# Kernel optimization log

Hardware: AMD Instinct MI355X
Metric: run time of the kernel (lower is better)

Reference implementation:

```python
import jax, jax.numpy as jnp
import numpy as np

B, NA, D, H = 64, 32, 128, 6  # scenes, agents/scene, out_dim, heads
N = B * NA
E = B * NA * NA


def layer_norm(x, g, b, eps=1e-5):
    m = jnp.mean(x, axis=-1, keepdims=True)
    v = jnp.var(x, axis=-1, keepdims=True)
    return (x - m) * jax.lax.rsqrt(v + eps) * g + b


def setup_inputs() -> dict:
    key = jax.random.key(0)
    ks = jax.random.split(key, 10)
    # fully-connected edges within each scene
    ids = jnp.arange(N, dtype=jnp.int32).reshape(B, NA)
    hi = jnp.broadcast_to(ids[:, :, None], (B, NA, NA)).reshape(-1)  # repeat 'd -> (d n)'
    wi = jnp.broadcast_to(ids[:, None, :], (B, NA, NA)).reshape(-1)  # repeat 'd -> (n d)'
    s_in = 1.0 / np.sqrt(D)
    s_hd = 1.0 / np.sqrt(H * D)
    return {
        'agents': jax.random.normal(ks[0], (N, D), jnp.float32),
        'hi': hi, 'wi': wi,
        'Wq': jax.random.normal(ks[1], (H * D, D), jnp.float32) * s_in,
        'gq': jnp.ones((H * D,), jnp.float32), 'bq': jnp.zeros((H * D,), jnp.float32),
        'Wk': jax.random.normal(ks[2], (H * D, D), jnp.float32) * s_in,
        'gk': jnp.ones((H * D,), jnp.float32), 'bk': jnp.zeros((H * D,), jnp.float32),
        'Wv': jax.random.normal(ks[3], (H * D, D), jnp.float32) * s_in,
        'gv': jnp.ones((H * D,), jnp.float32), 'bv': jnp.zeros((H * D,), jnp.float32),
        'Wo1': jax.random.normal(ks[4], (D, H * D), jnp.float32) * s_hd,
        'go': jnp.ones((D,), jnp.float32), 'bo': jnp.zeros((D,), jnp.float32),
        'Wo2': jax.random.normal(ks[5], (D, D), jnp.float32) * s_in,
        'W1': jax.random.normal(ks[6], (D, D), jnp.float32) * s_in,
        'gn': jnp.ones((D,), jnp.float32), 'bn': jnp.zeros((D,), jnp.float32),
        'W2': jax.random.normal(ks[7], (D, D), jnp.float32) * s_in,
    }


def reference(agents, hi, wi, Wq, gq, bq, Wk, gk, bk, Wv, gv, bv, Wo1, go, bo, Wo2, W1, gn, bn, W2):
    n, d = agents.shape
    scale = d ** -0.5
    xh = agents[hi]                                   # [E, D]
    xw = agents[wi]                                   # [E, D]
    q = layer_norm(xh @ Wq.T, gq, bq).reshape(-1, H, d)                 # [E, H, D]
    k = layer_norm(xw @ Wk.T, gk, bk).reshape(-1, H, d)
    v = jax.nn.relu(layer_norm(xw @ Wv.T, gv, bv)).reshape(-1, H, d)
    att = jnp.sum(q * k, axis=-1) * scale             # [E, H] per-edge score
    att = jnp.exp(att - jnp.max(att))                 # global max, as in original
    att_sum = jax.ops.segment_sum(att, hi, num_segments=n)   # [N, H]
    att = att / att_sum[hi]
    out = jax.ops.segment_sum(att[..., None] * v, hi, num_segments=n)   # [N, H, D]
    out = out.reshape(n, H * d)
    out = jax.nn.relu(layer_norm(out @ Wo1.T, go, bo)) @ Wo2.T          # to_out
    nodes = agents @ W1.T
    nodes = jax.nn.relu(layer_norm(nodes + out, gn, bn))
    nodes = nodes @ W2.T
    return jax.nn.relu(nodes + agents)
```

## Files before the change

### kernel.cpp

```cpp
#include <hip/hip_runtime.h>
#include <math.h>

#define NN 2048
#define HH 6
#define HD 768
#define NA 32
#define NB 64

typedef __bf16 bf16x8 __attribute__((ext_vector_type(8)));
typedef float  f32x4  __attribute__((ext_vector_type(4)));

__device__ __forceinline__ void split2(float f, ushort& h, ushort& l) {
    const uint u = __float_as_uint(f);
    h = (ushort)(u >> 16);
    const float hf = __uint_as_float((uint)h << 16);
    l = (ushort)(__float_as_uint(f - hf) >> 16);
}

__device__ __forceinline__ bf16x8 pack8(const ushort* s) {
    uint4 u;
    u.x = (uint)s[0] | ((uint)s[1] << 16);
    u.y = (uint)s[2] | ((uint)s[3] << 16);
    u.z = (uint)s[4] | ((uint)s[5] << 16);
    u.w = (uint)s[6] | ((uint)s[7] << 16);
    return *(bf16x8*)&u;
}

__device__ __forceinline__ void ln8_split(
    const float* __restrict__ x, float mu, float rs,
    const float* __restrict__ g, const float* __restrict__ b,
    bf16x8& hi, bf16x8& lo)
{
    const float4 x0 = *(const float4*)x;
    const float4 x1 = *(const float4*)(x + 4);
    const float4 g0 = *(const float4*)g;
    const float4 g1 = *(const float4*)(g + 4);
    const float4 b0 = *(const float4*)b;
    const float4 b1 = *(const float4*)(b + 4);
    ushort hh[8], ll[8];
    float v;
    v = (x0.x - mu) * rs * g0.x + b0.x; split2(v, hh[0], ll[0]);
    v = (x0.y - mu) * rs * g0.y + b0.y; split2(v, hh[1], ll[1]);
    v = (x0.z - mu) * rs * g0.z + b0.z; split2(v, hh[2], ll[2]);
    v = (x0.w - mu) * rs * g0.w + b0.w; split2(v, hh[3], ll[3]);
    v = (x1.x - mu) * rs * g1.x + b1.x; split2(v, hh[4], ll[4]);
    v = (x1.y - mu) * rs * g1.y + b1.y; split2(v, hh[5], ll[5]);
    v = (x1.z - mu) * rs * g1.z + b1.z; split2(v, hh[6], ll[6]);
    v = (x1.w - mu) * rs * g1.w + b1.w; split2(v, hh[7], ll[7]);
    hi = pack8(hh); lo = pack8(ll);
}

__global__ __launch_bounds__(256) void split_kernel(
    const float* __restrict__ agents, const float* __restrict__ Wq,
    const float* __restrict__ Wk, const float* __restrict__ Wv,
    const float* __restrict__ Wo1, const float* __restrict__ Wo2,
    const float* __restrict__ W1, const float* __restrict__ W2,
    ushort* __restrict__ Ahi, ushort* __restrict__ Alo,
    ushort* __restrict__ Whi, ushort* __restrict__ Wlo,
    ushort* __restrict__ Wo1hi, ushort* __restrict__ Wo1lo,
    ushort* __restrict__ Wo2hi, ushort* __restrict__ Wo2lo,
    ushort* __restrict__ W1hi, ushort* __restrict__ W1lo,
    ushort* __restrict__ W2hi, ushort* __restrict__ W2lo)
{
    const int y = blockIdx.y;
    const float* src;
    ushort *dh, *dl;
    int n4;
    switch (y) {
        case 0:  src = agents; dh = Ahi;   dl = Alo;   n4 = NN * 128 / 4;  break;
        case 1:  src = Wq;  dh = Whi;                dl = Wlo;                n4 = 768*128/4; break;
        case 2:  src = Wk;  dh = Whi + 768*128;      dl = Wlo + 768*128;      n4 = 768*128/4; break;
        case 3:  src = Wv;  dh = Whi + 2*768*128;    dl = Wlo + 2*768*128;    n4 = 768*128/4; break;
        case 4:  src = Wo1; dh = Wo1hi; dl = Wo1lo;  n4 = 128 * HD / 4;  break;
        case 5:  src = Wo2; dh = Wo2hi; dl = Wo2lo;  n4 = 128 * 128 / 4; break;
        case 6:  src = W1;  dh = W1hi;  dl = W1lo;   n4 = 128 * 128 / 4; break;
        default: src = W2;  dh = W2hi;  dl = W2lo;   n4 = 128 * 128 / 4; break;
    }
    const int i = blockIdx.x * 256 + threadIdx.x;
    if (i < n4) {
        const float4 v = ((const float4*)src)[i];
        ushort4 h, l;
        split2(v.x, h.x, l.x);
        split2(v.y, h.y, l.y);
        split2(v.z, h.z, l.z);
        split2(v.w, h.w, l.w);
        ((ushort4*)dh)[i] = h;
        ((ushort4*)dl)[i] = l;
    }
}

__global__ __launch_bounds__(256) void proj_mfma_kernel(
    const ushort* __restrict__ Ahi, const ushort* __restrict__ Alo,
    const ushort* __restrict__ Whi, const ushort* __restrict__ Wlo,
    float* __restrict__ R)
{
    const int tid = threadIdx.x;
    const int wave = tid >> 6, lane = tid & 63;
    const int row0 = blockIdx.x * 64 + wave * 16;
    const int cb0  = blockIdx.y * 64;
    const int lrow = lane & 15, kq = lane >> 4;
    const int koff = kq * 8;

    const ushort* ah = Ahi + (size_t)(row0 + lrow) * 128 + koff;
    const ushort* al = Alo + (size_t)(row0 + lrow) * 128 + koff;

    f32x4 acc[4];
    #pragma unroll
    for (int ct = 0; ct < 4; ++ct)
        #pragma unroll
        for (int j = 0; j < 4; ++j) acc[ct][j] = 0.f;

    #pragma unroll
    for (int kt = 0; kt < 4; ++kt) {
        const bf16x8 avh = *(const bf16x8*)(ah + kt * 32);
        const bf16x8 avl = *(const bf16x8*)(al + kt * 32);
        #pragma unroll
        for (int ct = 0; ct < 4; ++ct) {
            const size_t wof = (size_t)(cb0 + ct * 16 + lrow) * 128 + koff + kt * 32;
            const bf16x8 bvh = *(const bf16x8*)(Whi + wof);
            const bf16x8 bvl = *(const bf16x8*)(Wlo + wof);
            acc[ct] = __builtin_amdgcn_mfma_f32_16x16x32_bf16(avh, bvh, acc[ct], 0, 0, 0);
            acc[ct] = __builtin_amdgcn_mfma_f32_16x16x32_bf16(avh, bvl, acc[ct], 0, 0, 0);
            acc[ct] = __builtin_amdgcn_mfma_f32_16x16x32_bf16(avl, bvh, acc[ct], 0, 0, 0);
        }
    }

    #pragma unroll
    for (int ct = 0; ct < 4; ++ct) {
        const int colg = cb0 + ct * 16;
        const int m = colg / 768;
        const int c = colg - m * 768 + lrow;
        float* rp = R + ((size_t)m * NN + row0 + kq * 4) * HD + c;
        #pragma unroll
        for (int j = 0; j < 4; ++j)
            rp[(size_t)j * HD] = acc[ct][j];
    }
}

__global__ __launch_bounds__(256) void stats_kernel(
    const float* __restrict__ R, float* __restrict__ ps)
{
    const int wave = threadIdx.x >> 6, lane = threadIdx.x & 63;
    const int rr = blockIdx.x * 4 + wave;
    const float4* rp = (const float4*)(R + (size_t)rr * HD);
    float s = 0.f, q = 0.f;
    #pragma unroll
    for (int r = 0; r < 3; ++r) {
        const float4 v = rp[lane + r * 64];
        s += v.x + v.y + v.z + v.w;
        q += v.x * v.x + v.y * v.y + v.z * v.z + v.w * v.w;
    }
    #pragma unroll
    for (int mask = 32; mask >= 1; mask >>= 1) {
        s += __shfl_xor(s, mask);
        q += __shfl_xor(q, mask);
    }
    if (lane == 0) { ps[(size_t)rr * 2] = s; ps[(size_t)rr * 2 + 1] = q; }
}

__global__ __launch_bounds__(64) void attn_mfma_kernel(
    const float* __restrict__ R, const float* __restrict__ ps,
    const float* __restrict__ gq, const float* __restrict__ bq,
    const float* __restrict__ gk, const float* __restrict__ bk,
    const float* __restrict__ gv, const float* __restrict__ bv,
    ushort* __restrict__ Ohi, ushort* __restrict__ Olo)
{
    __shared__ ushort phi[16][40];
    __shared__ ushort plo[16][40];
    const int lane = threadIdx.x;
    const int lrow = lane & 15, kq = lane >> 4;
    const int scene = blockIdx.x, h = blockIdx.y, rt = blockIdx.z;
    const int brow = scene * 32;

    const float* Rq = R;
    const float* Rk = R + (size_t)NN * HD;
    const float* Rv = R + (size_t)2 * NN * HD;

    const int qrow = brow + rt * 16 + lrow;
    const float2 sq_ = *(const float2*)(ps + (size_t)qrow * 2);
    const float muq = sq_.x * (1.f / 768.f);
    const float rsq = rsqrtf(sq_.y * (1.f / 768.f) - muq * muq + 1e-5f);

    float muk[2], rsk[2];
    #pragma unroll
    for (int ct = 0; ct < 2; ++ct) {
        const int krow = brow + ct * 16 + lrow;
        const float2 sk_ = *(const float2*)(ps + (size_t)(NN + krow) * 2);
        muk[ct] = sk_.x * (1.f / 768.f);
        rsk[ct] = rsqrtf(sk_.y * (1.f / 768.f) - muk[ct] * muk[ct] + 1e-5f);
    }
    float muv[8], rsv[8];
    #pragma unroll
    for (int j = 0; j < 8; ++j) {
        const int vrow = brow + kq * 8 + j;
        const float2 sv_ = *(const float2*)(ps + (size_t)(2 * NN + vrow) * 2);
        muv[j] = sv_.x * (1.f / 768.f);
        rsv[j] = rsqrtf(sv_.y * (1.f / 768.f) - muv[j] * muv[j] + 1e-5f);
    }

    f32x4 s[2];
    #pragma unroll
    for (int ct = 0; ct < 2; ++ct)
        #pragma unroll
        for (int j = 0; j < 4; ++j) s[ct][j] = 0.f;

    #pragma unroll
    for (int kt = 0; kt < 4; ++kt) {
        const int c0 = h * 128 + kt * 32 + kq * 8;
        bf16x8 qh, ql;
        ln8_split(Rq + (size_t)qrow * HD + c0, muq, rsq, gq + c0, bq + c0, qh, ql);
        #pragma unroll
        for (int ct = 0; ct < 2; ++ct) {
            bf16x8 kh, kl;
            ln8_split(Rk + (size_t)(brow + ct * 16 + lrow) * HD + c0, muk[ct], rsk[ct],
                      gk + c0, bk + c0, kh, kl);
            s[ct] = __builtin_amdgcn_mfma_f32_16x16x32_bf16(qh, kh, s[ct], 0, 0, 0);
            s[ct] = __builtin_amdgcn_mfma_f32_16x16x32_bf16(qh, kl, s[ct], 0, 0, 0);
            s[ct] = __builtin_amdgcn_mfma_f32_16x16x32_bf16(ql, kh, s[ct], 0, 0, 0);
        }
    }

    const float scl = 0.08838834764831845f;
    float p0[4], p1[4];
    #pragma unroll
    for (int j = 0; j < 4; ++j) {
        const float a = s[0][j] * scl, b = s[1][j] * scl;
        float m = fmaxf(a, b);
        #pragma unroll
        for (int msk = 1; msk <= 8; msk <<= 1) m = fmaxf(m, __shfl_xor(m, msk));
        const float ea = __expf(a - m), eb = __expf(b - m);
        float su = ea + eb;
        #pragma unroll
        for (int msk = 1; msk <= 8; msk <<= 1) su += __shfl_xor(su, msk);
        const float inv = 1.f / su;
        p0[j] = ea * inv;
        p1[j] = eb * inv;
    }

    #pragma unroll
    for (int j = 0; j < 4; ++j) {
        ushort hh, ll;
        split2(p0[j], hh, ll);
        phi[kq * 4 + j][lrow] = hh;
        plo[kq * 4 + j][lrow] = ll;
        split2(p1[j], hh, ll);
        phi[kq * 4 + j][16 + lrow] = hh;
        plo[kq * 4 + j][16 + lrow] = ll;
    }
    __syncthreads();
    const bf16x8 pah = *(const bf16x8*)&phi[lrow][kq * 8];
    const bf16x8 pal = *(const bf16x8*)&plo[lrow][kq * 8];

    #pragma unroll
    for (int dt = 0; dt < 8; ++dt) {
        const int d = h * 128 + dt * 16 + lrow;
        const float gvd = gv[d], bvd = bv[d];
        ushort vh[8], vl[8];
        #pragma unroll
        for (int j = 0; j < 8; ++j) {
            const float x = Rv[(size_t)(brow + kq * 8 + j) * HD + d];
            const float v = fmaxf((x - muv[j]) * rsv[j] * gvd + bvd, 0.f);
            split2(v, vh[j], vl[j]);
        }
        const bf16x8 bh = pack8(vh), bl = pack8(vl);
        f32x4 o;
        #pragma unroll
        for (int j = 0; j < 4; ++j) o[j] = 0.f;
        o = __builtin_amdgcn_mfma_f32_16x16x32_bf16(pah, bh, o, 0, 0, 0);
        o = __builtin_amdgcn_mfma_f32_16x16x32_bf16(pah, bl, o, 0, 0, 0);
        o = __builtin_amdgcn_mfma_f32_16x16x32_bf16(pal, bh, o, 0, 0, 0);
        #pragma unroll
        for (int j = 0; j < 4; ++j) {
            const size_t oo = (size_t)(brow + rt * 16 + kq * 4 + j) * HD + d;
            ushort hh, ll;
            split2(o[j], hh, ll);
            Ohi[oo] = hh;
            Olo[oo] = ll;
        }
    }
}

__global__ __launch_bounds__(256) void wo1_mfma_kernel(
    const ushort* __restrict__ Ohi, const ushort* __restrict__ Olo,
    const ushort* __restrict__ Wo1hi, const ushort* __restrict__ Wo1lo,
    float* __restrict__ P)
{
    const int tid = threadIdx.x;
    const int wave = tid >> 6, lane = tid & 63;
    const int row0 = blockIdx.x * 64 + wave * 16;
    const int col0 = blockIdx.y * 16;
    const int kb   = blockIdx.z * 256;
    const int lrow = lane & 15, kq = lane >> 4;
    const int koff = kq * 8;

    const ushort* ah = Ohi   + (size_t)(row0 + lrow) * HD + kb + koff;
    const ushort* al = Olo   + (size_t)(row0 + lrow) * HD + kb + koff;
    const ushort* bh = Wo1hi + (size_t)(col0 + lrow) * HD + kb + koff;
    const ushort* bl = Wo1lo + (size_t)(col0 + lrow) * HD + kb + koff;

    f32x4 acc;
    #pragma unroll
    for (int j = 0; j < 4; ++j) acc[j] = 0.f;

    #pragma unroll
    for (int kt = 0; kt < 8; ++kt) {
        const bf16x8 avh = *(const bf16x8*)(ah + kt * 32);
        const bf16x8 avl = *(const bf16x8*)(al + kt * 32);
        const bf16x8 bvh = *(const bf16x8*)(bh + kt * 32);
        const bf16x8 bvl = *(const bf16x8*)(bl + kt * 32);
        acc = __builtin_amdgcn_mfma_f32_16x16x32_bf16(avh, bvh, acc, 0, 0, 0);
        acc = __builtin_amdgcn_mfma_f32_16x16x32_bf16(avh, bvl, acc, 0, 0, 0);
        acc = __builtin_amdgcn_mfma_f32_16x16x32_bf16(avl, bvh, acc, 0, 0, 0);
    }

    float* pp = P + ((size_t)blockIdx.z * NN + row0 + kq * 4) * 128 + col0 + lrow;
    #pragma unroll
    for (int j = 0; j < 4; ++j)
        pp[(size_t)j * 128] = acc[j];
}

__global__ __launch_bounds__(64) void epilogue_mfma_kernel(
    const float* __restrict__ P,
    const ushort* __restrict__ Ahi, const ushort* __restrict__ Alo,
    const float* __restrict__ agents,
    const float* __restrict__ go, const float* __restrict__ bo,
    const ushort* __restrict__ Wo2hi, const ushort* __restrict__ Wo2lo,
    const ushort* __restrict__ W1hi, const ushort* __restrict__ W1lo,
    const float* __restrict__ gn, const float* __restrict__ bn,
    const ushort* __restrict__ W2hi, const ushort* __restrict__ W2lo,
    float* __restrict__ out)
{
    __shared__ float zb[16][132];
    const int lane = threadIdx.x;
    const int lrow = lane & 15, kq = lane >> 4;
    const int n0 = blockIdx.x * 16;
    const int nodeA = n0 + lrow;

    float tv[4][8];
    float s = 0.f, q = 0.f;
    #pragma unroll
    for (int kt = 0; kt < 4; ++kt) {
        const int c0 = kt * 32 + kq * 8;
        const float* pp0 = P + (size_t)nodeA * 128 + c0;
        const float* pp1 = pp0 + (size_t)NN * 128;
        const float* pp2 = pp1 + (size_t)NN * 128;
        #pragma unroll
        for (int hf = 0; hf < 2; ++hf) {
            const float4 a = *(const float4*)(pp0 + hf * 4);
            const float4 b = *(const float4*)(pp1 + hf * 4);
            const float4 c = *(const float4*)(pp2 + hf * 4);
            tv[kt][hf * 4 + 0] = a.x + b.x + c.x;
            tv[kt][hf * 4 + 1] = a.y + b.y + c.y;
            tv[kt][hf * 4 + 2] = a.z + b.z + c.z;
            tv[kt][hf * 4 + 3] = a.w + b.w + c.w;
        }
        #pragma unroll
        for (int j = 0; j < 8; ++j) { s += tv[kt][j]; q += tv[kt][j] * tv[kt][j]; }
    }
    s += __shfl_xor(s, 16); s += __shfl_xor(s, 32);
    q += __shfl_xor(q, 16); q += __shfl_xor(q, 32);
    const float mu = s * (1.f / 128.f);
    const float rs = rsqrtf(q * (1.f / 128.f) - mu * mu + 1e-5f);

    bf16x8 th[4], tl[4], ah[4], al[4];
    #pragma unroll
    for (int kt = 0; kt < 4; ++kt) {
        const int c0 = kt * 32 + kq * 8;
        const float4 g0 = *(const float4*)(go + c0);
        const float4 g1 = *(const float4*)(go + c0 + 4);
        const float4 b0 = *(const float4*)(bo + c0);
        const float4 b1 = *(const float4*)(bo + c0 + 4);
        const float gg[8] = {g0.x, g0.y, g0.z, g0.w, g1.x, g1.y, g1.z, g1.w};
        const float bb[8] = {b0.x, b0.y, b0.z, b0.w, b1.x, b1.y, b1.z, b1.w};
        ushort hh[8], ll[8];
        #pragma unroll
        for (int j = 0; j < 8; ++j) {
            const float v = fmaxf((tv[kt][j] - mu) * rs * gg[j] + bb[j], 0.f);
            split2(v, hh[j], ll[j]);
        }
        th[kt] = pack8(hh); tl[kt] = pack8(ll);
        ah[kt] = *(const bf16x8*)(Ahi + (size_t)nodeA * 128 + c0);
        al[kt] = *(const bf16x8*)(Alo + (size_t)nodeA * 128 + c0);
    }

    f32x4 u[8];
    #pragma unroll
    for (int ct = 0; ct < 8; ++ct)
        #pragma unroll
        for (int j = 0; j < 4; ++j) u[ct][j] = 0.f;

    #pragma unroll
    for (int ct = 0; ct < 8; ++ct) {
        const size_t wb = (size_t)(ct * 16 + lrow) * 128;
        #pragma unroll
        for (int kt = 0; kt < 4; ++kt) {
            const int c0 = kt * 32 + kq * 8;
            const bf16x8 wh = *(const bf16x8*)(Wo2hi + wb + c0);
            const bf16x8 wl = *(const bf16x8*)(Wo2lo + wb + c0);
            const bf16x8 vh = *(const bf16x8*)(W1hi + wb + c0);
            const bf16x8 vl = *(const bf16x8*)(W1lo + wb + c0);
            u[ct] = __builtin_amdgcn_mfma_f32_16x16x32_bf16(th[kt], wh, u[ct], 0, 0, 0);
            u[ct] = __builtin_amdgcn_mfma_f32_16x16x32_bf16(th[kt], wl, u[ct], 0, 0, 0);
            u[ct] = __builtin_amdgcn_mfma_f32_16x16x32_bf16(tl[kt], wh, u[ct], 0, 0, 0);
            u[ct] = __builtin_amdgcn_mfma_f32_16x16x32_bf16(ah[kt], vh, u[ct], 0, 0, 0);
            u[ct] = __builtin_amdgcn_mfma_f32_16x16x32_bf16(ah[kt], vl, u[ct], 0, 0, 0);
            u[ct] = __builtin_amdgcn_mfma_f32_16x16x32_bf16(al[kt], vh, u[ct], 0, 0, 0);
        }
    }

    float gnc[8], bnc[8];
    #pragma unroll
    for (int ct = 0; ct < 8; ++ct) {
        gnc[ct] = gn[ct * 16 + lrow];
        bnc[ct] = bn[ct * 16 + lrow];
    }
    #pragma unroll
    for (int j = 0; j < 4; ++j) {
        float s2 = 0.f, q2 = 0.f;
        #pragma unroll
        for (int ct = 0; ct < 8; ++ct) { const float v = u[ct][j]; s2 += v; q2 += v * v; }
        #pragma unroll
        for (int msk = 1; msk <= 8; msk <<= 1) {
            s2 += __shfl_xor(s2, msk);
            q2 += __shfl_xor(q2, msk);
        }
        const float mu2 = s2 * (1.f / 128.f);
        const float rs2 = rsqrtf(q2 * (1.f / 128.f) - mu2 * mu2 + 1e-5f);
        #pragma unroll
        for (int ct = 0; ct < 8; ++ct)
            zb[kq * 4 + j][ct * 16 + lrow] =
                fmaxf((u[ct][j] - mu2) * rs2 * gnc[ct] + bnc[ct], 0.f);
    }
    __syncthreads();

    bf16x8 zh[4], zl[4];
    #pragma unroll
    for (int kt = 0; kt < 4; ++kt) {
        const int c0 = kt * 32 + kq * 8;
        const float4 z0 = *(const float4*)&zb[lrow][c0];
        const float4 z1 = *(const float4*)&zb[lrow][c0 + 4];
        const float zz[8] = {z0.x, z0.y, z0.z, z0.w, z1.x, z1.y, z1.z, z1.w};
        ushort hh[8], ll[8];
        #pragma unroll
        for (int j = 0; j < 8; ++j) split2(zz[j], hh[j], ll[j]);
        zh[kt] = pack8(hh); zl[kt] = pack8(ll);
    }
    #pragma unroll
    for (int ct = 0; ct < 8; ++ct) {
        f32x4 o;
        #pragma unroll
        for (int j = 0; j < 4; ++j) o[j] = 0.f;
        const size_t wb = (size_t)(ct * 16 + lrow) * 128;
        #pragma unroll
        for (int kt = 0; kt < 4; ++kt) {
            const int c0 = kt * 32 + kq * 8;
            const bf16x8 wh = *(const bf16x8*)(W2hi + wb + c0);
            const bf16x8 wl = *(const bf16x8*)(W2lo + wb + c0);
            o = __builtin_amdgcn_mfma_f32_16x16x32_bf16(zh[kt], wh, o, 0, 0, 0);
            o = __builtin_amdgcn_mfma_f32_16x16x32_bf16(zh[kt], wl, o, 0, 0, 0);
            o = __builtin_amdgcn_mfma_f32_16x16x32_bf16(zl[kt], wh, o, 0, 0, 0);
        }
        #pragma unroll
        for (int j = 0; j < 4; ++j) {
            const size_t oo = (size_t)(n0 + kq * 4 + j) * 128 + ct * 16 + lrow;
            out[oo] = fmaxf(o[j] + agents[oo], 0.f);
        }
    }
}

extern "C" void kernel_launch(void* const* d_in, const int* in_sizes, int n_in,
                              void* d_out, int out_size, void* d_ws, size_t ws_size,
                              hipStream_t stream) {
    (void)in_sizes; (void)n_in; (void)out_size; (void)ws_size;
    const float* agents = (const float*)d_in[0];
    const float* Wq  = (const float*)d_in[3];
    const float* gq  = (const float*)d_in[4];
    const float* bq  = (const float*)d_in[5];
    const float* Wk  = (const float*)d_in[6];
    const float* gk  = (const float*)d_in[7];
    const float* bk  = (const float*)d_in[8];
    const float* Wv  = (const float*)d_in[9];
    const float* gv  = (const float*)d_in[10];
    const float* bv  = (const float*)d_in[11];
    const float* Wo1 = (const float*)d_in[12];
    const float* go  = (const float*)d_in[13];
    const float* bo  = (const float*)d_in[14];
    const float* Wo2 = (const float*)d_in[15];
    const float* W1  = (const float*)d_in[16];
    const float* gn  = (const float*)d_in[17];
    const float* bn  = (const float*)d_in[18];
    const float* W2  = (const float*)d_in[19];
    float* out = (float*)d_out;

    float* ws = (float*)d_ws;
    float* R  = ws;
    float* Pp = R;
    float* ps = R + (size_t)3 * NN * HD;
    ushort* u = (ushort*)(ps + (size_t)2 * 3 * NN);
    ushort* Ohi   = u;  u += (size_t)NN * HD;
    ushort* Olo   = u;  u += (size_t)NN * HD;
    ushort* Ahi   = u;  u += (size_t)NN * 128;
    ushort* Alo   = u;  u += (size_t)NN * 128;
    ushort* Whi   = u;  u += (size_t)3 * 768 * 128;
    ushort* Wlo   = u;  u += (size_t)3 * 768 * 128;
    ushort* Wo1hi = u;  u += (size_t)128 * HD;
    ushort* Wo1lo = u;  u += (size_t)128 * HD;
    ushort* Wo2hi = u;  u += (size_t)128 * 128;
    ushort* Wo2lo = u;  u += (size_t)128 * 128;
    ushort* W1hi  = u;  u += (size_t)128 * 128;
    ushort* W1lo  = u;  u += (size_t)128 * 128;
    ushort* W2hi  = u;  u += (size_t)128 * 128;
    ushort* W2lo  = u;  u += (size_t)128 * 128;

    split_kernel<<<dim3(256, 8), 256, 0, stream>>>(
        agents, Wq, Wk, Wv, Wo1, Wo2, W1, W2,
        Ahi, Alo, Whi, Wlo, Wo1hi, Wo1lo, Wo2hi, Wo2lo, W1hi, W1lo, W2hi, W2lo);
    proj_mfma_kernel<<<dim3(32, 36), 256, 0, stream>>>(Ahi, Alo, Whi, Wlo, R);
    stats_kernel<<<1536, 256, 0, stream>>>(R, ps);
    attn_mfma_kernel<<<dim3(64, 6, 2), 64, 0, stream>>>(R, ps, gq, bq, gk, bk, gv, bv, Ohi, Olo);
    wo1_mfma_kernel<<<dim3(32, 8, 3), 256, 0, stream>>>(Ohi, Olo, Wo1hi, Wo1lo, Pp);
    epilogue_mfma_kernel<<<128, 64, 0, stream>>>(Pp, Ahi, Alo, agents, go, bo,
                                                 Wo2hi, Wo2lo, W1hi, W1lo, gn, bn,
                                                 W2hi, W2lo, out);
}
```

Measured before the change: 170.8 us.

## Fuse LayerNorm statistics into projection GEMM and widen epilogue to four waves

The projection GEMM now writes per-row partial sums and sums of squares for each 64-column block into a 24-slot buffer. This removes the separate stats kernel, which re-read the full 3×2048×768 projection output. The attention kernel reduces those 12 partials per row into shared memory before use. The epilogue kernel also moves from one wave to four waves per block, each computing a quarter of the output columns, with a shared-memory cross-wave LayerNorm reduction. The cost is extra shuffles and partial stores in the GEMM plus more synchronisation in the epilogue.

```diff
diff --git a/kernel.cpp b/kernel.cpp
--- a/kernel.cpp
+++ b/kernel.cpp
@@ -92,12 +92,13 @@
 __global__ __launch_bounds__(256) void proj_mfma_kernel(
     const ushort* __restrict__ Ahi, const ushort* __restrict__ Alo,
     const ushort* __restrict__ Whi, const ushort* __restrict__ Wlo,
-    float* __restrict__ R)
+    float* __restrict__ R, float* __restrict__ ps)
 {
     const int tid = threadIdx.x;
     const int wave = tid >> 6, lane = tid & 63;
     const int row0 = blockIdx.x * 64 + wave * 16;
     const int cb0  = blockIdx.y * 64;
+    const int m0   = blockIdx.y / 12, pb = blockIdx.y % 12;
     const int lrow = lane & 15, kq = lane >> 4;
     const int koff = kq * 8;
 
@@ -125,37 +126,32 @@
         }
     }
 
+    const int cloc = cb0 - m0 * 768;
     #pragma unroll
     for (int ct = 0; ct < 4; ++ct) {
-        const int colg = cb0 + ct * 16;
-        const int m = colg / 768;
-        const int c = colg - m * 768 + lrow;
-        float* rp = R + ((size_t)m * NN + row0 + kq * 4) * HD + c;
+        const int c = cloc + ct * 16 + lrow;
+        float* rp = R + ((size_t)m0 * NN + row0 + kq * 4) * HD + c;
         #pragma unroll
         for (int j = 0; j < 4; ++j)
             rp[(size_t)j * HD] = acc[ct][j];
     }
-}
-
-__global__ __launch_bounds__(256) void stats_kernel(
-    const float* __restrict__ R, float* __restrict__ ps)
-{
-    const int wave = threadIdx.x >> 6, lane = threadIdx.x & 63;
-    const int rr = blockIdx.x * 4 + wave;
-    const float4* rp = (const float4*)(R + (size_t)rr * HD);
-    float s = 0.f, q = 0.f;
-    #pragma unroll
-    for (int r = 0; r < 3; ++r) {
-        const float4 v = rp[lane + r * 64];
-        s += v.x + v.y + v.z + v.w;
-        q += v.x * v.x + v.y * v.y + v.z * v.z + v.w * v.w;
-    }
-    #pragma unroll
-    for (int mask = 32; mask >= 1; mask >>= 1) {
-        s += __shfl_xor(s, mask);
-        q += __shfl_xor(q, mask);
-    }
-    if (lane == 0) { ps[(size_t)rr * 2] = s; ps[(size_t)rr * 2 + 1] = q; }
+
+    #pragma unroll
+    for (int j = 0; j < 4; ++j) {
+        float sj = acc[0][j] + acc[1][j] + acc[2][j] + acc[3][j];
+        float qj = acc[0][j] * acc[0][j] + acc[1][j] * acc[1][j]
+                 + acc[2][j] * acc[2][j] + acc[3][j] * acc[3][j];
+        #pragma unroll
+        for (int msk = 1; msk <= 8; msk <<= 1) {
+            sj += __shfl_xor(sj, msk);
+            qj += __shfl_xor(qj, msk);
+        }
+        if (lrow == 0) {
+            const size_t o = ((size_t)m0 * NN + row0 + kq * 4 + j) * 24 + pb * 2;
+            ps[o]     = sj;
+            ps[o + 1] = qj;
+        }
+    }
 }
 
 __global__ __launch_bounds__(64) void attn_mfma_kernel(
@@ -167,6 +163,7 @@
 {
     __shared__ ushort phi[16][40];
     __shared__ ushort plo[16][40];
+    __shared__ float stat_s[3][32][2];
     const int lane = threadIdx.x;
     const int lrow = lane & 15, kq = lane >> 4;
     const int scene = blockIdx.x, h = blockIdx.y, rt = blockIdx.z;
@@ -176,26 +173,37 @@
     const float* Rk = R + (size_t)NN * HD;
     const float* Rv = R + (size_t)2 * NN * HD;
 
+    for (int i = lane; i < 96; i += 64) {
+        const int m = i >> 5, row = i & 31;
+        const float4* pv = (const float4*)(ps + ((size_t)m * NN + brow + row) * 24);
+        float s = 0.f, q = 0.f;
+        #pragma unroll
+        for (int c = 0; c < 6; ++c) {
+            const float4 v = pv[c];
+            s += v.x + v.z;
+            q += v.y + v.w;
+        }
+        const float mu  = s * (1.f / 768.f);
+        const float var = q * (1.f / 768.f) - mu * mu;
+        stat_s[m][row][0] = mu;
+        stat_s[m][row][1] = rsqrtf(var + 1e-5f);
+    }
+    __syncthreads();
+
     const int qrow = brow + rt * 16 + lrow;
-    const float2 sq_ = *(const float2*)(ps + (size_t)qrow * 2);
-    const float muq = sq_.x * (1.f / 768.f);
-    const float rsq = rsqrtf(sq_.y * (1.f / 768.f) - muq * muq + 1e-5f);
-
+    const float muq = stat_s[0][rt * 16 + lrow][0];
+    const float rsq = stat_s[0][rt * 16 + lrow][1];
     float muk[2], rsk[2];
     #pragma unroll
     for (int ct = 0; ct < 2; ++ct) {
-        const int krow = brow + ct * 16 + lrow;
-        const float2 sk_ = *(const float2*)(ps + (size_t)(NN + krow) * 2);
-        muk[ct] = sk_.x * (1.f / 768.f);
-        rsk[ct] = rsqrtf(sk_.y * (1.f / 768.f) - muk[ct] * muk[ct] + 1e-5f);
+        muk[ct] = stat_s[1][ct * 16 + lrow][0];
+        rsk[ct] = stat_s[1][ct * 16 + lrow][1];
     }
     float muv[8], rsv[8];
     #pragma unroll
     for (int j = 0; j < 8; ++j) {
-        const int vrow = brow + kq * 8 + j;
-        const float2 sv_ = *(const float2*)(ps + (size_t)(2 * NN + vrow) * 2);
-        muv[j] = sv_.x * (1.f / 768.f);
-        rsv[j] = rsqrtf(sv_.y * (1.f / 768.f) - muv[j] * muv[j] + 1e-5f);
+        muv[j] = stat_s[2][kq * 8 + j][0];
+        rsv[j] = stat_s[2][kq * 8 + j][1];
     }
 
     f32x4 s[2];
@@ -319,7 +327,7 @@
         pp[(size_t)j * 128] = acc[j];
 }
 
-__global__ __launch_bounds__(64) void epilogue_mfma_kernel(
+__global__ __launch_bounds__(256) void epilogue_mfma_kernel(
     const float* __restrict__ P,
     const ushort* __restrict__ Ahi, const ushort* __restrict__ Alo,
     const float* __restrict__ agents,
@@ -331,7 +339,9 @@
     float* __restrict__ out)
 {
     __shared__ float zb[16][132];
-    const int lane = threadIdx.x;
+    __shared__ float red2[4][16][2];
+    const int tid = threadIdx.x;
+    const int wave = tid >> 6, lane = tid & 63;
     const int lrow = lane & 15, kq = lane >> 4;
     const int n0 = blockIdx.x * 16;
     const int nodeA = n0 + lrow;
@@ -383,14 +393,15 @@
         al[kt] = *(const bf16x8*)(Alo + (size_t)nodeA * 128 + c0);
     }
 
-    f32x4 u[8];
-    #pragma unroll
-    for (int ct = 0; ct < 8; ++ct)
-        #pragma unroll
-        for (int j = 0; j < 4; ++j) u[ct][j] = 0.f;
-
-    #pragma unroll
-    for (int ct = 0; ct < 8; ++ct) {
+    f32x4 u[2];
+    #pragma unroll
+    for (int ct2 = 0; ct2 < 2; ++ct2)
+        #pragma unroll
+        for (int j = 0; j < 4; ++j) u[ct2][j] = 0.f;
+
+    #pragma unroll
+    for (int ct2 = 0; ct2 < 2; ++ct2) {
+        const int ct = wave * 2 + ct2;
         const size_t wb = (size_t)(ct * 16 + lrow) * 128;
         #pragma unroll
         for (int kt = 0; kt < 4; ++kt) {
@@ -399,37 +410,42 @@
             const bf16x8 wl = *(const bf16x8*)(Wo2lo + wb + c0);
             const bf16x8 vh = *(const bf16x8*)(W1hi + wb + c0);
             const bf16x8 vl = *(const bf16x8*)(W1lo + wb + c0);
-            u[ct] = __builtin_amdgcn_mfma_f32_16x16x32_bf16(th[kt], wh, u[ct], 0, 0, 0);
-            u[ct] = __builtin_amdgcn_mfma_f32_16x16x32_bf16(th[kt], wl, u[ct], 0, 0, 0);
-            u[ct] = __builtin_amdgcn_mfma_f32_16x16x32_bf16(tl[kt], wh, u[ct], 0, 0, 0);
-            u[ct] = __builtin_amdgcn_mfma_f32_16x16x32_bf16(ah[kt], vh, u[ct], 0, 0, 0);
-            u[ct] = __builtin_amdgcn_mfma_f32_16x16x32_bf16(ah[kt], vl, u[ct], 0, 0, 0);
-            u[ct] = __builtin_amdgcn_mfma_f32_16x16x32_bf16(al[kt], vh, u[ct], 0, 0, 0);
-        }
-    }
-
-    float gnc[8], bnc[8];
-    #pragma unroll
-    for (int ct = 0; ct < 8; ++ct) {
-        gnc[ct] = gn[ct * 16 + lrow];
-        bnc[ct] = bn[ct * 16 + lrow];
-    }
+            u[ct2] = __builtin_amdgcn_mfma_f32_16x16x32_bf16(th[kt], wh, u[ct2], 0, 0, 0);
+            u[ct2] = __builtin_amdgcn_mfma_f32_16x16x32_bf16(th[kt], wl, u[ct2], 0, 0, 0);
+            u[ct2] = __builtin_amdgcn_mfma_f32_16x16x32_bf16(tl[kt], wh, u[ct2], 0, 0, 0);
+            u[ct2] = __builtin_amdgcn_mfma_f32_16x16x32_bf16(ah[kt], vh, u[ct2], 0, 0, 0);
+            u[ct2] = __builtin_amdgcn_mfma_f32_16x16x32_bf16(ah[kt], vl, u[ct2], 0, 0, 0);
+            u[ct2] = __builtin_amdgcn_mfma_f32_16x16x32_bf16(al[kt], vh, u[ct2], 0, 0, 0);
+        }
+    }
+
     #pragma unroll
     for (int j = 0; j < 4; ++j) {
-        float s2 = 0.f, q2 = 0.f;
-        #pragma unroll
-        for (int ct = 0; ct < 8; ++ct) { const float v = u[ct][j]; s2 += v; q2 += v * v; }
+        float s2 = u[0][j] + u[1][j];
+        float q2 = u[0][j] * u[0][j] + u[1][j] * u[1][j];
         #pragma unroll
         for (int msk = 1; msk <= 8; msk <<= 1) {
             s2 += __shfl_xor(s2, msk);
             q2 += __shfl_xor(q2, msk);
         }
-        const float mu2 = s2 * (1.f / 128.f);
-        const float rs2 = rsqrtf(q2 * (1.f / 128.f) - mu2 * mu2 + 1e-5f);
-        #pragma unroll
-        for (int ct = 0; ct < 8; ++ct)
-            zb[kq * 4 + j][ct * 16 + lrow] =
-                fmaxf((u[ct][j] - mu2) * rs2 * gnc[ct] + bnc[ct], 0.f);
+        if (lrow == 0) {
+            red2[wave][kq * 4 + j][0] = s2;
+            red2[wave][kq * 4 + j][1] = q2;
+        }
+    }
+    __syncthreads();
+    #pragma unroll
+    for (int j = 0; j < 4; ++j) {
+        const int row = kq * 4 + j;
+        const float s2t = red2[0][row][0] + red2[1][row][0] + red2[2][row][0] + red2[3][row][0];
+        const float q2t = red2[0][row][1] + red2[1][row][1] + red2[2][row][1] + red2[3][row][1];
+        const float mu2 = s2t * (1.f / 128.f);
+        const float rs2 = rsqrtf(q2t * (1.f / 128.f) - mu2 * mu2 + 1e-5f);
+        #pragma unroll
+        for (int ct2 = 0; ct2 < 2; ++ct2) {
+            const int c = (wave * 2 + ct2) * 16 + lrow;
+            zb[row][c] = fmaxf((u[ct2][j] - mu2) * rs2 * gn[c] + bn[c], 0.f);
+        }
     }
     __syncthreads();
 
@@ -446,7 +462,8 @@
         zh[kt] = pack8(hh); zl[kt] = pack8(ll);
     }
     #pragma unroll
-    for (int ct = 0; ct < 8; ++ct) {
+    for (int ct2 = 0; ct2 < 2; ++ct2) {
+        const int ct = wave * 2 + ct2;
         f32x4 o;
         #pragma unroll
         for (int j = 0; j < 4; ++j) o[j] = 0.f;
@@ -496,7 +513,7 @@
     float* R  = ws;
     float* Pp = R;
     float* ps = R + (size_t)3 * NN * HD;
-    ushort* u = (ushort*)(ps + (size_t)2 * 3 * NN);
+    ushort* u = (ushort*)(ps + (size_t)3 * NN * 24);
     ushort* Ohi   = u;  u += (size_t)NN * HD;
     ushort* Olo   = u;  u += (size_t)NN * HD;
     ushort* Ahi   = u;  u += (size_t)NN * 128;
@@ -515,11 +532,10 @@
     split_kernel<<<dim3(256, 8), 256, 0, stream>>>(
         agents, Wq, Wk, Wv, Wo1, Wo2, W1, W2,
         Ahi, Alo, Whi, Wlo, Wo1hi, Wo1lo, Wo2hi, Wo2lo, W1hi, W1lo, W2hi, W2lo);
-    proj_mfma_kernel<<<dim3(32, 36), 256, 0, stream>>>(Ahi, Alo, Whi, Wlo, R);
-    stats_kernel<<<1536, 256, 0, stream>>>(R, ps);
+    proj_mfma_kernel<<<dim3(32, 36), 256, 0, stream>>>(Ahi, Alo, Whi, Wlo, R, ps);
     attn_mfma_kernel<<<dim3(64, 6, 2), 64, 0, stream>>>(R, ps, gq, bq, gk, bk, gv, bv, Ohi, Olo);
     wo1_mfma_kernel<<<dim3(32, 8, 3), 256, 0, stream>>>(Ohi, Olo, Wo1hi, Wo1lo, Pp);
-    epilogue_mfma_kernel<<<128, 64, 0, stream>>>(Pp, Ahi, Alo, agents, go, bo,
-                                                 Wo2hi, Wo2lo, W1hi, W1lo, gn, bn,
-                                                 W2hi, W2lo, out);
-}
+    epilogue_mfma_kernel<<<128, 256, 0, stream>>>(Pp, Ahi, Alo, agents, go, bo,
+                                                  Wo2hi, Wo2lo, W1hi, W1lo, gn, bn,
+                                                  W2hi, W2lo, out);
+}
```

Result: faster. 160.4 us (-6.1%).
